# Optimization experiments

Hardware: AMD Instinct MI355X
Metric: run time of the kernel (lower is better)

The kernel has to match this reference:

```python
import jax, jax.numpy as jnp
import numpy as np

B, N, P, D = 16, 1024, 72, 96
ND, H, K = 64, 4, 16
LN_EPS = 1e-5
ROW_EPS = 1e-8


def topk_sparsify(adj, k):
    # adj: (..., N, N); keep top-k per row (scatter-mask), then row-renormalize
    shp = adj.shape
    n = shp[-1]
    flat = adj.reshape(-1, n)
    _, idx = jax.lax.top_k(flat, k)  # (R, k)
    rows = jnp.arange(flat.shape[0])[:, None]
    mask = jnp.zeros_like(flat).at[rows, idx].set(1.0)
    sp = flat * mask
    sp = sp / (sp.sum(-1, keepdims=True) + ROW_EPS)
    return sp.reshape(shp)


def setup_inputs() -> dict:
    key = jax.random.key(0)
    ks = jax.random.split(key, 12)
    xav1 = np.sqrt(6.0 / (N + ND))  # xavier_uniform bound for (N, ND)
    inp = {
        "patch_features": jax.random.normal(ks[0], (B, N, P, D), jnp.float32),
        "E1": jax.random.uniform(ks[1], (H, N, ND), jnp.float32, -xav1, xav1),
        "E2": jax.random.uniform(ks[2], (H, ND, N), jnp.float32, -xav1, xav1),
        "temperature": jnp.full((H,), 0.5, jnp.float32),
        "fusion_weight": jnp.float32(0.5),
        "dW1": jax.random.normal(ks[3], (D, ND), jnp.float32) / np.sqrt(D),
        "db1": jnp.zeros((ND,), jnp.float32),
        "ln_g": jnp.ones((ND,), jnp.float32),
        "ln_b": jnp.zeros((ND,), jnp.float32),
        "dW2": jax.random.normal(ks[4], (ND, ND), jnp.float32) / np.sqrt(ND),
        "db2": jnp.zeros((ND,), jnp.float32),
        "eW1": jax.random.normal(ks[5], (H, 2 * H), jnp.float32) / np.sqrt(H),
        "eb1": jnp.zeros((2 * H,), jnp.float32),
        "eW2": jax.random.normal(ks[6], (2 * H, 1), jnp.float32) / np.sqrt(2 * H),
        "eb2": jnp.zeros((1,), jnp.float32),
    }
    return inp


def reference(patch_features, E1, E2, temperature, fusion_weight,
              dW1, db1, ln_g, ln_b, dW2, db2, eW1, eb1, eW2, eb2):
    # ---- static multi-head graphs: softmax(relu(E1 @ E2) / T, axis=-1) ----
    s = jax.nn.relu(jnp.einsum('hnd,hdm->hnm', E1, E2))
    static_adjs = jax.nn.softmax(s / temperature[:, None, None], axis=-1)

    # ---- dynamic graphs from mean-pooled patch features ----
    node_repr = patch_features.mean(axis=2)                 # (B, N, D)
    h1 = node_repr @ dW1 + db1                              # (B, N, ND)
    mu = h1.mean(-1, keepdims=True)
    var = ((h1 - mu) ** 2).mean(-1, keepdims=True)
    h1 = (h1 - mu) / jnp.sqrt(var + LN_EPS) * ln_g + ln_b   # LayerNorm
    h1 = jax.nn.relu(h1)                                    # (dropout = identity, eval)
    dyn_emb = h1 @ dW2 + db2                                # (B, N, ND)
    d = jax.nn.relu(jnp.einsum('bnd,hdm->bhnm', dyn_emb, E2))
    dynamic_adjs = jax.nn.softmax(d / temperature[None, :, None, None], axis=-1)

    # ---- top-k sparsify + row renormalize ----
    static_adjs = topk_sparsify(static_adjs, K)             # (H, N, N)
    dynamic_adjs = topk_sparsify(dynamic_adjs, K)           # (B, H, N, N)

    # ---- fuse static + dynamic ----
    fused = (1.0 - fusion_weight) * static_adjs[None] + fusion_weight * dynamic_adjs

    # ---- edge MLP over head dim: (B, N, N, H) -> (B, N, N) ----
    x = jnp.transpose(fused, (0, 2, 3, 1))                  # (B, N, N, H)
    ew = jax.nn.relu(x @ eW1 + eb1) @ eW2 + eb2             # (B, N, N, 1)
    final_adjs = jax.nn.sigmoid(ew[..., 0]) * fused.mean(axis=1)
    return final_adjs, static_adjs, dynamic_adjs
```

## Files before the change

kernel.cpp:

```cpp
#include <hip/hip_runtime.h>

typedef unsigned int u32;
typedef unsigned long long u64;
typedef unsigned short u16;

#define Bn 16
#define Nn 1024
#define Pp 72
#define MARG 3e-4f

#define NEGINF __int_as_float(0xff800000)
#define POSINF __int_as_float(0x7f800000)

#define DPP_STEP(OP, CTRL, RM)                                                 \
  y = __builtin_amdgcn_update_dpp(__float_as_int(v), __float_as_int(v),        \
                                  CTRL, RM, 0xf, false);                       \
  v = OP(v, __int_as_float(y));

#define DPP_RED(NAME, OP)                                                      \
  __device__ __forceinline__ float NAME(float v) {                             \
    int y;                                                                     \
    DPP_STEP(OP, 0x111, 0xf)                                                   \
    DPP_STEP(OP, 0x112, 0xf)                                                   \
    DPP_STEP(OP, 0x114, 0xf)                                                   \
    DPP_STEP(OP, 0x118, 0xf)                                                   \
    DPP_STEP(OP, 0x142, 0xa)                                                   \
    DPP_STEP(OP, 0x143, 0xc)                                                   \
    return __int_as_float(__builtin_amdgcn_readlane(__float_as_int(v), 63));   \
  }

#define FADDOP(a, b) ((a) + (b))
DPP_RED(dmaxf, fmaxf)
DPP_RED(dminf, fminf)
DPP_RED(dsumf, FADDOP)

__device__ __forceinline__ u32 wminu(u32 v) {
#pragma unroll
  for (int off = 1; off < 64; off <<= 1) {
    u32 o = (u32)__shfl_xor((int)v, off, 64);
    v = (o < v) ? o : v;
  }
  return v;
}

__global__ __launch_bounds__(256) void k_e2t(const float* __restrict__ E2,
                                             float* __restrict__ E2T) {
  __shared__ float tile[32][65];
  const int h = blockIdx.x >> 5;
  const int m0 = (blockIdx.x & 31) << 5;
  const float* src = E2 + (size_t)h * 65536;
  float* dst = E2T + (size_t)h * 65536;
  const int t = threadIdx.x;
#pragma unroll
  for (int k = 0; k < 8; ++k) {
    int idx = k * 256 + t;
    int d = idx >> 5, mm = idx & 31;
    tile[mm][d] = src[d * 1024 + m0 + mm];
  }
  __syncthreads();
#pragma unroll
  for (int k = 0; k < 8; ++k) {
    int idx = k * 256 + t;
    int mm = idx >> 6, d = idx & 63;
    dst[(size_t)(m0 + mm) * 64 + d] = tile[mm][d];
  }
}

__global__ __launch_bounds__(128) void k_meanmlp(const float* __restrict__ pf,
                                                 const float* __restrict__ dW1,
                                                 const float* __restrict__ db1,
                                                 const float* __restrict__ ln_g,
                                                 const float* __restrict__ ln_b,
                                                 const float* __restrict__ dW2,
                                                 const float* __restrict__ db2,
                                                 double* __restrict__ embD,
                                                 float* __restrict__ embF) {
  __shared__ double ndD[96];
  __shared__ double red[64];
  __shared__ double h1r[64];
  const int t = threadIdx.x;
  const int bn = blockIdx.x;

  if (t < 96) {
    const float* src = pf + (size_t)bn * (Pp * 96) + t;
    double s = 0.0;
    for (int p = 0; p < Pp; ++p) s += (double)src[p * 96];
    ndD[t] = s / 72.0;
  }
  __syncthreads();

  double a = 0.0;
  if (t < 64) {
    a = (double)db1[t];
    for (int d = 0; d < 96; ++d) a = fma(ndD[d], (double)dW1[d * 64 + t], a);
    red[t] = a;
  }
  __syncthreads();
  for (int s2 = 32; s2 >= 1; s2 >>= 1) {
    if (t < s2) red[t] += red[t + s2];
    __syncthreads();
  }
  const double mu = red[0] * (1.0 / 64.0);
  __syncthreads();
  const double dv = a - mu;
  if (t < 64) red[t] = dv * dv;
  __syncthreads();
  for (int s2 = 32; s2 >= 1; s2 >>= 1) {
    if (t < s2) red[t] += red[t + s2];
    __syncthreads();
  }
  const double var = red[0] * (1.0 / 64.0);
  if (t < 64) {
    double xn = dv / sqrt(var + 1e-5) * (double)ln_g[t] + (double)ln_b[t];
    h1r[t] = xn > 0.0 ? xn : 0.0;
  }
  __syncthreads();
  if (t < 64) {
    double e = (double)db2[t];
    for (int k = 0; k < 64; ++k) e = fma(h1r[k], (double)dW2[k * 64 + t], e);
    embD[(size_t)bn * 64 + t] = e;
    embF[(size_t)bn * 64 + t] = (float)e;
  }
}

template <int MODE>
__global__ __launch_bounds__(512) void k_dot(const float* __restrict__ e1f,
                                             const float* __restrict__ embF,
                                             const float* __restrict__ E2,
                                             const float* __restrict__ temp,
                                             float* __restrict__ outp) {
  __shared__ float embsh[64][16];
  const int t = threadIdx.x;
  const int r0 = blockIdx.x * 16;
  int h;
  size_t erow;
  if (MODE == 0) {
    h = r0 >> 10;
    erow = (size_t)r0;
  } else {
    int b = r0 >> 12;
    h = (r0 >> 10) & 3;
    int n0 = r0 & 1023;
    erow = (size_t)(b << 10) + n0;
  }
  const float* efa = (MODE == 0) ? (e1f + erow * 64) : (embF + erow * 64);
  const float2* e2 = (const float2*)(E2 + (size_t)h * 65536);
  const float invT = 1.0f / temp[h];

#pragma unroll
  for (int i = t; i < 1024; i += 512) {
    int g = i & 15, d = i >> 4;
    embsh[d][g] = efa[g * 64 + d];
  }
  __syncthreads();

  float acc[16][2];
#pragma unroll
  for (int g = 0; g < 16; ++g) { acc[g][0] = 0.0f; acc[g][1] = 0.0f; }

#define FMA2(g, s)                                                             \
  acc[g][0] = fmaf(s, ev.x, acc[g][0]);                                        \
  acc[g][1] = fmaf(s, ev.y, acc[g][1]);

#pragma unroll 2
  for (int d = 0; d < 64; ++d) {
    float2 ev = e2[d * 512 + t];
    float4 sa = *(const float4*)&embsh[d][0];
    float4 sb = *(const float4*)&embsh[d][4];
    float4 sc = *(const float4*)&embsh[d][8];
    float4 sd = *(const float4*)&embsh[d][12];
    FMA2(0, sa.x) FMA2(1, sa.y) FMA2(2, sa.z) FMA2(3, sa.w)
    FMA2(4, sb.x) FMA2(5, sb.y) FMA2(6, sb.z) FMA2(7, sb.w)
    FMA2(8, sc.x) FMA2(9, sc.y) FMA2(10, sc.z) FMA2(11, sc.w)
    FMA2(12, sd.x) FMA2(13, sd.y) FMA2(14, sd.z) FMA2(15, sd.w)
  }
#undef FMA2

#pragma unroll
  for (int g = 0; g < 16; ++g) {
    float2 o;
    o.x = fmaxf(acc[g][0], 0.0f) * invT;
    o.y = fmaxf(acc[g][1], 0.0f) * invT;
    ((float2*)(outp + (size_t)(r0 + g) * 1024))[t] = o;
  }
}

template <int MODE>
__global__ __launch_bounds__(256) void k_sel(const float* __restrict__ e1f,
                                             const double* __restrict__ embD,
                                             const float* __restrict__ E2T,
                                             const float* __restrict__ temp,
                                             float* __restrict__ outp) {
  const int t = threadIdx.x;
  const int w = t >> 6, l = t & 63;
  const int r = blockIdx.x * 4 + w;
  int h;
  size_t erow;
  if (MODE == 0) {
    h = r >> 10;
    erow = (size_t)r;
  } else {
    int b = r >> 12;
    h = (r >> 10) & 3;
    int n = r & 1023;
    erow = (size_t)(b << 10) + n;
  }
  const float* e2t = E2T + (size_t)h * 65536;
  const double Td = (double)temp[h];
  float* row = outp + (size_t)r * 1024;

  float q[16];
#pragma unroll
  for (int j = 0; j < 16; ++j) q[j] = row[l + (j << 6)];

  float lm = q[0];
#pragma unroll
  for (int j = 1; j < 16; ++j) lm = fmaxf(lm, q[j]);
  const float qmax = dmaxf(lm);

  u32 lo = 0u, hi = __float_as_uint(qmax) + 1u;
  u32 kept = 0u;
  bool f16 = false;
  float pvf = 0.0f;
#pragma unroll 1
  while (hi - lo > 1u) {
    u32 mid = (lo + hi) >> 1;
    float pv = __uint_as_float(mid);
    u32 cw = 0;
#pragma unroll
    for (int j = 0; j < 16; ++j)
      cw += (u32)__popcll(__ballot(q[j] >= pv));
    if (cw >= 16u) lo = mid; else hi = mid;
    if (cw == 16u) { f16 = true; pvf = pv; break; }
  }
  float theta, ub;
  if (f16) {
    float vmin = POSINF, umax = -1.0f;
#pragma unroll
    for (int j = 0; j < 16; ++j) {
      if (q[j] >= pvf) { kept |= 1u << j; vmin = fminf(vmin, q[j]); }
      else umax = fmaxf(umax, q[j]);
    }
    theta = dminf(vmin);
    ub = dmaxf(umax);
  } else {
    theta = __uint_as_float(lo);
    u32 cw = 0;
#pragma unroll
    for (int j = 0; j < 16; ++j) {
      cw += (u32)__popcll(__ballot(q[j] > theta));
      if (q[j] > theta) kept |= 1u << j;
    }
    int rr = 16 - (int)cw;
#pragma unroll 1
    for (int it = 0; it < rr; ++it) {
      u32 mc = 0xFFFFFFFFu;
#pragma unroll
      for (int j = 0; j < 16; ++j)
        if (q[j] == theta && !((kept >> j) & 1u)) {
          u32 cc = (u32)((j << 6) | l);
          mc = cc < mc ? cc : mc;
        }
      u32 wm = wminu(mc);
      if ((wm & 63u) == (u32)l) kept |= 1u << (wm >> 6);
    }
    ub = theta;
  }

  if (theta - ub >= MARG) {
    float e[16];
    float es = 0.0f, ek = 0.0f;
#pragma unroll
    for (int j = 0; j < 16; ++j) {
      e[j] = __expf(q[j] - qmax);
      es += e[j];
      if ((kept >> j) & 1u) ek += e[j];
    }
    const float Z = dsumf(es);
    const float EK = dsumf(ek);
    const float inv = 1.0f / (EK + 1e-8f * Z);
#pragma unroll
    for (int j = 0; j < 16; ++j)
      row[l + (j << 6)] = ((kept >> j) & 1u) ? (e[j] * inv) : 0.0f;
  } else {
    double qd[16];
    const float thr = ub - MARG;
#pragma unroll 1
    for (int j = 0; j < 16; ++j) {
      if (q[j] >= thr) {
        const int m = l + (j << 6);
        const float* col = e2t + (size_t)m * 64;
        double a = 0.0;
        for (int d = 0; d < 64; ++d) {
          double s = (MODE == 0) ? (double)e1f[erow * 64 + d]
                                 : embD[erow * 64 + d];
          a = fma(s, (double)col[d], a);
        }
        qd[j] = (a > 0.0 ? a : 0.0) / Td;
      } else {
        qd[j] = (double)q[j];
      }
    }
    double bm = qd[0];
#pragma unroll
    for (int j = 1; j < 16; ++j) bm = qd[j] > bm ? qd[j] : bm;
    float mh = (float)bm;
    float mlo = (float)(bm - (double)mh);
    float whi = dmaxf(mh);
    float wlo = dmaxf(mh == whi ? mlo : NEGINF);
    const double qmaxd = (double)whi + (double)wlo;

    float ev2[16];
    float es2 = 0.0f;
#pragma unroll
    for (int j = 0; j < 16; ++j) { ev2[j] = __expf((float)(qd[j] - qmaxd)); es2 += ev2[j]; }
    const float Z2 = dsumf(es2);

    u32 kept2 = 0;
    float EK2 = 0.0f;
#pragma unroll 1
    for (int it = 0; it < 16; ++it) {
      double bv = -1.0;
      int bjj = -1;
#pragma unroll
      for (int j = 0; j < 16; ++j) {
        bool tk = (((kept2 >> j) & 1u) == 0u) && (qd[j] > bv);
        bv = tk ? qd[j] : bv;
        bjj = tk ? j : bjj;
      }
      float bh = NEGINF, bl = NEGINF;
      if (bjj >= 0) { bh = (float)bv; bl = (float)(bv - (double)bh); }
      float vhi = dmaxf(bh);
      float vlo = dmaxf(bh == vhi ? bl : NEGINF);
      bool elig = (bh == vhi) && (bl == vlo);
      u32 mc = elig ? (u32)((bjj << 6) | l) : 0xFFFFFFFFu;
      u32 mwin = wminu(mc);
      EK2 += __expf((float)(((double)vhi + (double)vlo) - qmaxd));
      if ((mwin & 63u) == (u32)l) kept2 |= 1u << (mwin >> 6);
    }
    const float inv2 = 1.0f / (EK2 + 1e-8f * Z2);
#pragma unroll
    for (int j = 0; j < 16; ++j)
      row[l + (j << 6)] = ((kept2 >> j) & 1u) ? (ev2[j] * inv2) : 0.0f;
  }
}

__global__ __launch_bounds__(256) void k_fuse(const float* __restrict__ dyn,
                                              const float* __restrict__ stat,
                                              float* __restrict__ fin,
                                              const float* __restrict__ eW1,
                                              const float* __restrict__ eb1,
                                              const float* __restrict__ eW2,
                                              const float* __restrict__ eb2,
                                              const float* __restrict__ fwp) {
  const float w = fwp[0];
  const float w1 = 1.0f - w;
  float W1[4][8], B1v[8], W2v[8];
#pragma unroll
  for (int hh = 0; hh < 4; ++hh)
#pragma unroll
    for (int j = 0; j < 8; ++j) W1[hh][j] = eW1[hh * 8 + j];
#pragma unroll
  for (int j = 0; j < 8; ++j) { B1v[j] = eb1[j]; W2v[j] = eW2[j]; }
  const float b2 = eb2[0];

  const int i = blockIdx.x * 256 + threadIdx.x;
  const int b = i >> 18;
  const int rem = i & 262143;
  const int n = rem >> 8;
  const int c4 = rem & 255;

  float fx[4][4];
#pragma unroll
  for (int hh = 0; hh < 4; ++hh) {
    float4 fd = ((const float4*)dyn)[(((size_t)((b * 4 + hh) * 1024 + n)) << 8) + c4];
    float4 fs = ((const float4*)stat)[(((size_t)(hh * 1024 + n)) << 8) + c4];
    fx[hh][0] = w1 * fs.x + w * fd.x;
    fx[hh][1] = w1 * fs.y + w * fd.y;
    fx[hh][2] = w1 * fs.z + w * fd.z;
    fx[hh][3] = w1 * fs.w + w * fd.w;
  }
  float ov[4];
#pragma unroll
  for (int x = 0; x < 4; ++x) {
    float ew = b2;
#pragma unroll
    for (int j = 0; j < 8; ++j) {
      float hj = B1v[j];
#pragma unroll
      for (int hh = 0; hh < 4; ++hh) hj = fmaf(fx[hh][x], W1[hh][j], hj);
      ew = fmaf(fmaxf(hj, 0.0f), W2v[j], ew);
    }
    float mean = (fx[0][x] + fx[1][x] + fx[2][x] + fx[3][x]) * 0.25f;
    float sg = 1.0f / (1.0f + __expf(-ew));
    ov[x] = sg * mean;
  }
  float4 o;
  o.x = ov[0]; o.y = ov[1]; o.z = ov[2]; o.w = ov[3];
  ((float4*)fin)[i] = o;
}

extern "C" void kernel_launch(void* const* d_in, const int* in_sizes, int n_in,
                              void* d_out, int out_size, void* d_ws, size_t ws_size,
                              hipStream_t stream) {
  const float* pf   = (const float*)d_in[0];
  const float* E1   = (const float*)d_in[1];
  const float* E2   = (const float*)d_in[2];
  const float* temp = (const float*)d_in[3];
  const float* fw   = (const float*)d_in[4];
  const float* dW1  = (const float*)d_in[5];
  const float* db1  = (const float*)d_in[6];
  const float* ln_g = (const float*)d_in[7];
  const float* ln_b = (const float*)d_in[8];
  const float* dW2  = (const float*)d_in[9];
  const float* db2  = (const float*)d_in[10];
  const float* eW1  = (const float*)d_in[11];
  const float* eb1  = (const float*)d_in[12];
  const float* eW2  = (const float*)d_in[13];
  const float* eb2  = (const float*)d_in[14];

  float* out_final = (float*)d_out;
  float* out_stat  = out_final + (size_t)Bn * Nn * Nn;
  float* out_dyn   = out_stat + (size_t)4 * Nn * Nn;

  double* embD = (double*)d_out;
  float* embF = out_final + 2097152;
  float* E2T  = out_final + 3145728;

  k_e2t<<<128, 256, 0, stream>>>(E2, E2T);
  k_meanmlp<<<Bn * Nn, 128, 0, stream>>>(pf, dW1, db1, ln_g, ln_b, dW2, db2, embD, embF);
  k_dot<0><<<256, 512, 0, stream>>>(E1, nullptr, E2, temp, out_stat);
  k_sel<0><<<1024, 256, 0, stream>>>(E1, nullptr, E2T, temp, out_stat);
  k_dot<1><<<4096, 512, 0, stream>>>(nullptr, embF, E2, temp, out_dyn);
  k_sel<1><<<16384, 256, 0, stream>>>(nullptr, embD, E2T, temp, out_dyn);
  k_fuse<<<16384, 256, 0, stream>>>(out_dyn, out_stat, out_final, eW1, eb1, eW2, eb2, fw);
}
```

Before: 588.9 us.

## Fuse dynamic top-k selection with edge-MLP fusion and retile dot kernel

Merges the dynamic-graph selection kernel and the fusion/edge-MLP kernel into one block per (b,n). The block processes all four head rows, keeps the sparsified rows in shared memory and uses them directly for the fused output. This saves one full read of the 256MB dynamic tensor. The dot kernel is retiled to 256 threads, each computing an 8x8 register tile with float4 loads. Scratch buffers move from the output region to the workspace.

```diff
diff --git a/kernel.cpp b/kernel.cpp
--- a/kernel.cpp
+++ b/kernel.cpp
@@ -2,7 +2,6 @@
 
 typedef unsigned int u32;
 typedef unsigned long long u64;
-typedef unsigned short u16;
 
 #define Bn 16
 #define Nn 1024
@@ -41,6 +40,144 @@
     v = (o < v) ? o : v;
   }
   return v;
+}
+
+template <int MODE>
+__device__ __forceinline__ void select_row(const float* __restrict__ q,
+                                           float* __restrict__ v, int l,
+                                           const float* __restrict__ e1row,
+                                           const double* __restrict__ edrow,
+                                           const float* __restrict__ e2t,
+                                           double Td) {
+  float lm = q[0];
+#pragma unroll
+  for (int j = 1; j < 16; ++j) lm = fmaxf(lm, q[j]);
+  const float qmax = dmaxf(lm);
+
+  u32 lo = 0u, hi = __float_as_uint(qmax) + 1u;
+  u32 kept = 0u;
+  bool f16 = false;
+  float pvf = 0.0f;
+#pragma unroll 1
+  while (hi - lo > 1u) {
+    u32 mid = (lo + hi) >> 1;
+    float pv = __uint_as_float(mid);
+    u32 cw = 0;
+#pragma unroll
+    for (int j = 0; j < 16; ++j)
+      cw += (u32)__popcll(__ballot(q[j] >= pv));
+    if (cw >= 16u) lo = mid; else hi = mid;
+    if (cw == 16u) { f16 = true; pvf = pv; break; }
+  }
+  float theta, ub;
+  if (f16) {
+    float vmin = POSINF, umax = -1.0f;
+#pragma unroll
+    for (int j = 0; j < 16; ++j) {
+      if (q[j] >= pvf) { kept |= 1u << j; vmin = fminf(vmin, q[j]); }
+      else umax = fmaxf(umax, q[j]);
+    }
+    theta = dminf(vmin);
+    ub = dmaxf(umax);
+  } else {
+    theta = __uint_as_float(lo);
+    u32 cw = 0;
+#pragma unroll
+    for (int j = 0; j < 16; ++j) {
+      cw += (u32)__popcll(__ballot(q[j] > theta));
+      if (q[j] > theta) kept |= 1u << j;
+    }
+    int rr = 16 - (int)cw;
+#pragma unroll 1
+    for (int it = 0; it < rr; ++it) {
+      u32 mc = 0xFFFFFFFFu;
+#pragma unroll
+      for (int j = 0; j < 16; ++j)
+        if (q[j] == theta && !((kept >> j) & 1u)) {
+          u32 cc = (u32)((j << 6) | l);
+          mc = cc < mc ? cc : mc;
+        }
+      u32 wm = wminu(mc);
+      if ((wm & 63u) == (u32)l) kept |= 1u << (wm >> 6);
+    }
+    ub = theta;
+  }
+
+  if (theta - ub >= MARG) {
+    float e[16];
+    float es = 0.0f, ek = 0.0f;
+#pragma unroll
+    for (int j = 0; j < 16; ++j) {
+      e[j] = __expf(q[j] - qmax);
+      es += e[j];
+      if ((kept >> j) & 1u) ek += e[j];
+    }
+    const float Z = dsumf(es);
+    const float EK = dsumf(ek);
+    const float inv = 1.0f / (EK + 1e-8f * Z);
+#pragma unroll
+    for (int j = 0; j < 16; ++j)
+      v[j] = ((kept >> j) & 1u) ? (e[j] * inv) : 0.0f;
+  } else {
+    double qd[16];
+    const float thr = ub - MARG;
+#pragma unroll 1
+    for (int j = 0; j < 16; ++j) {
+      if (q[j] >= thr) {
+        const int m = l + (j << 6);
+        const float* col = e2t + (size_t)m * 64;
+        double a = 0.0;
+        for (int d = 0; d < 64; ++d) {
+          double s = (MODE == 0) ? (double)e1row[d] : edrow[d];
+          a = fma(s, (double)col[d], a);
+        }
+        qd[j] = (a > 0.0 ? a : 0.0) / Td;
+      } else {
+        qd[j] = (double)q[j];
+      }
+    }
+    double bm = qd[0];
+#pragma unroll
+    for (int j = 1; j < 16; ++j) bm = qd[j] > bm ? qd[j] : bm;
+    float mh = (float)bm;
+    float mlo = (float)(bm - (double)mh);
+    float whi = dmaxf(mh);
+    float wlo = dmaxf(mh == whi ? mlo : NEGINF);
+    const double qmaxd = (double)whi + (double)wlo;
+
+    float ev2[16];
+    float es2 = 0.0f;
+#pragma unroll
+    for (int j = 0; j < 16; ++j) { ev2[j] = __expf((float)(qd[j] - qmaxd)); es2 += ev2[j]; }
+    const float Z2 = dsumf(es2);
+
+    u32 kept2 = 0;
+    float EK2 = 0.0f;
+#pragma unroll 1
+    for (int it = 0; it < 16; ++it) {
+      double bv = -1.0;
+      int bjj = -1;
+#pragma unroll
+      for (int j = 0; j < 16; ++j) {
+        bool tk = (((kept2 >> j) & 1u) == 0u) && (qd[j] > bv);
+        bv = tk ? qd[j] : bv;
+        bjj = tk ? j : bjj;
+      }
+      float bh = NEGINF, bl = NEGINF;
+      if (bjj >= 0) { bh = (float)bv; bl = (float)(bv - (double)bh); }
+      float vhi = dmaxf(bh);
+      float vlo = dmaxf(bh == vhi ? bl : NEGINF);
+      bool elig = (bh == vhi) && (bl == vlo);
+      u32 mc = elig ? (u32)((bjj << 6) | l) : 0xFFFFFFFFu;
+      u32 mwin = wminu(mc);
+      EK2 += __expf((float)(((double)vhi + (double)vlo) - qmaxd));
+      if ((mwin & 63u) == (u32)l) kept2 |= 1u << (mwin >> 6);
+    }
+    const float inv2 = 1.0f / (EK2 + 1e-8f * Z2);
+#pragma unroll
+    for (int j = 0; j < 16; ++j)
+      v[j] = ((kept2 >> j) & 1u) ? (ev2[j] * inv2) : 0.0f;
+  }
 }
 
 __global__ __launch_bounds__(256) void k_e2t(const float* __restrict__ E2,
@@ -124,7 +261,7 @@
 }
 
 template <int MODE>
-__global__ __launch_bounds__(512) void k_dot(const float* __restrict__ e1f,
+__global__ __launch_bounds__(256) void k_dot(const float* __restrict__ e1f,
                                              const float* __restrict__ embF,
                                              const float* __restrict__ E2,
                                              const float* __restrict__ temp,
@@ -144,217 +281,126 @@
     erow = (size_t)(b << 10) + n0;
   }
   const float* efa = (MODE == 0) ? (e1f + erow * 64) : (embF + erow * 64);
-  const float2* e2 = (const float2*)(E2 + (size_t)h * 65536);
+  const float* e2 = E2 + (size_t)h * 65536;
   const float invT = 1.0f / temp[h];
 
 #pragma unroll
-  for (int i = t; i < 1024; i += 512) {
+  for (int i = t; i < 1024; i += 256) {
     int g = i & 15, d = i >> 4;
     embsh[d][g] = efa[g * 64 + d];
   }
   __syncthreads();
 
-  float acc[16][2];
-#pragma unroll
-  for (int g = 0; g < 16; ++g) { acc[g][0] = 0.0f; acc[g][1] = 0.0f; }
-
-#define FMA2(g, s)                                                             \
-  acc[g][0] = fmaf(s, ev.x, acc[g][0]);                                        \
-  acc[g][1] = fmaf(s, ev.y, acc[g][1]);
-
-#pragma unroll 2
+  const int s = t >> 7;
+  const int c1 = (t & 127) * 4;
+  const int c2 = c1 + 512;
+
+  float acc[8][8];
+#pragma unroll
+  for (int g = 0; g < 8; ++g)
+#pragma unroll
+    for (int x = 0; x < 8; ++x) acc[g][x] = 0.0f;
+
+#pragma unroll 4
   for (int d = 0; d < 64; ++d) {
-    float2 ev = e2[d * 512 + t];
-    float4 sa = *(const float4*)&embsh[d][0];
-    float4 sb = *(const float4*)&embsh[d][4];
-    float4 sc = *(const float4*)&embsh[d][8];
-    float4 sd = *(const float4*)&embsh[d][12];
-    FMA2(0, sa.x) FMA2(1, sa.y) FMA2(2, sa.z) FMA2(3, sa.w)
-    FMA2(4, sb.x) FMA2(5, sb.y) FMA2(6, sb.z) FMA2(7, sb.w)
-    FMA2(8, sc.x) FMA2(9, sc.y) FMA2(10, sc.z) FMA2(11, sc.w)
-    FMA2(12, sd.x) FMA2(13, sd.y) FMA2(14, sd.z) FMA2(15, sd.w)
-  }
-#undef FMA2
-
-#pragma unroll
-  for (int g = 0; g < 16; ++g) {
-    float2 o;
-    o.x = fmaxf(acc[g][0], 0.0f) * invT;
-    o.y = fmaxf(acc[g][1], 0.0f) * invT;
-    ((float2*)(outp + (size_t)(r0 + g) * 1024))[t] = o;
-  }
-}
-
-template <int MODE>
-__global__ __launch_bounds__(256) void k_sel(const float* __restrict__ e1f,
-                                             const double* __restrict__ embD,
-                                             const float* __restrict__ E2T,
-                                             const float* __restrict__ temp,
-                                             float* __restrict__ outp) {
+    float4 va = *(const float4*)(e2 + d * 1024 + c1);
+    float4 vb = *(const float4*)(e2 + d * 1024 + c2);
+    float4 ea = *(const float4*)&embsh[d][8 * s];
+    float4 eb = *(const float4*)&embsh[d][8 * s + 4];
+    float sg;
+#define ROWFMA(g, SS)                                                          \
+    sg = SS;                                                                   \
+    acc[g][0] = fmaf(sg, va.x, acc[g][0]);                                     \
+    acc[g][1] = fmaf(sg, va.y, acc[g][1]);                                     \
+    acc[g][2] = fmaf(sg, va.z, acc[g][2]);                                     \
+    acc[g][3] = fmaf(sg, va.w, acc[g][3]);                                     \
+    acc[g][4] = fmaf(sg, vb.x, acc[g][4]);                                     \
+    acc[g][5] = fmaf(sg, vb.y, acc[g][5]);                                     \
+    acc[g][6] = fmaf(sg, vb.z, acc[g][6]);                                     \
+    acc[g][7] = fmaf(sg, vb.w, acc[g][7]);
+    ROWFMA(0, ea.x) ROWFMA(1, ea.y) ROWFMA(2, ea.z) ROWFMA(3, ea.w)
+    ROWFMA(4, eb.x) ROWFMA(5, eb.y) ROWFMA(6, eb.z) ROWFMA(7, eb.w)
+#undef ROWFMA
+  }
+
+#pragma unroll
+  for (int g = 0; g < 8; ++g) {
+    float* orow = outp + (size_t)(r0 + 8 * s + g) * 1024;
+    float4 o1, o2;
+    o1.x = fmaxf(acc[g][0], 0.0f) * invT;
+    o1.y = fmaxf(acc[g][1], 0.0f) * invT;
+    o1.z = fmaxf(acc[g][2], 0.0f) * invT;
+    o1.w = fmaxf(acc[g][3], 0.0f) * invT;
+    o2.x = fmaxf(acc[g][4], 0.0f) * invT;
+    o2.y = fmaxf(acc[g][5], 0.0f) * invT;
+    o2.z = fmaxf(acc[g][6], 0.0f) * invT;
+    o2.w = fmaxf(acc[g][7], 0.0f) * invT;
+    *(float4*)(orow + c1) = o1;
+    *(float4*)(orow + c2) = o2;
+  }
+}
+
+__global__ __launch_bounds__(256) void k_sel0(const float* __restrict__ E1,
+                                              const float* __restrict__ E2T,
+                                              const float* __restrict__ temp,
+                                              float* __restrict__ outp) {
   const int t = threadIdx.x;
   const int w = t >> 6, l = t & 63;
   const int r = blockIdx.x * 4 + w;
-  int h;
-  size_t erow;
-  if (MODE == 0) {
-    h = r >> 10;
-    erow = (size_t)r;
-  } else {
-    int b = r >> 12;
-    h = (r >> 10) & 3;
-    int n = r & 1023;
-    erow = (size_t)(b << 10) + n;
-  }
+  const int h = r >> 10;
   const float* e2t = E2T + (size_t)h * 65536;
   const double Td = (double)temp[h];
   float* row = outp + (size_t)r * 1024;
 
-  float q[16];
+  float q[16], v[16];
 #pragma unroll
   for (int j = 0; j < 16; ++j) q[j] = row[l + (j << 6)];
-
-  float lm = q[0];
-#pragma unroll
-  for (int j = 1; j < 16; ++j) lm = fmaxf(lm, q[j]);
-  const float qmax = dmaxf(lm);
-
-  u32 lo = 0u, hi = __float_as_uint(qmax) + 1u;
-  u32 kept = 0u;
-  bool f16 = false;
-  float pvf = 0.0f;
-#pragma unroll 1
-  while (hi - lo > 1u) {
-    u32 mid = (lo + hi) >> 1;
-    float pv = __uint_as_float(mid);
-    u32 cw = 0;
-#pragma unroll
-    for (int j = 0; j < 16; ++j)
-      cw += (u32)__popcll(__ballot(q[j] >= pv));
-    if (cw >= 16u) lo = mid; else hi = mid;
-    if (cw == 16u) { f16 = true; pvf = pv; break; }
-  }
-  float theta, ub;
-  if (f16) {
-    float vmin = POSINF, umax = -1.0f;
-#pragma unroll
-    for (int j = 0; j < 16; ++j) {
-      if (q[j] >= pvf) { kept |= 1u << j; vmin = fminf(vmin, q[j]); }
-      else umax = fmaxf(umax, q[j]);
-    }
-    theta = dminf(vmin);
-    ub = dmaxf(umax);
-  } else {
-    theta = __uint_as_float(lo);
-    u32 cw = 0;
-#pragma unroll
-    for (int j = 0; j < 16; ++j) {
-      cw += (u32)__popcll(__ballot(q[j] > theta));
-      if (q[j] > theta) kept |= 1u << j;
-    }
-    int rr = 16 - (int)cw;
-#pragma unroll 1
-    for (int it = 0; it < rr; ++it) {
-      u32 mc = 0xFFFFFFFFu;
-#pragma unroll
-      for (int j = 0; j < 16; ++j)
-        if (q[j] == theta && !((kept >> j) & 1u)) {
-          u32 cc = (u32)((j << 6) | l);
-          mc = cc < mc ? cc : mc;
-        }
-      u32 wm = wminu(mc);
-      if ((wm & 63u) == (u32)l) kept |= 1u << (wm >> 6);
-    }
-    ub = theta;
-  }
-
-  if (theta - ub >= MARG) {
-    float e[16];
-    float es = 0.0f, ek = 0.0f;
-#pragma unroll
-    for (int j = 0; j < 16; ++j) {
-      e[j] = __expf(q[j] - qmax);
-      es += e[j];
-      if ((kept >> j) & 1u) ek += e[j];
-    }
-    const float Z = dsumf(es);
-    const float EK = dsumf(ek);
-    const float inv = 1.0f / (EK + 1e-8f * Z);
-#pragma unroll
-    for (int j = 0; j < 16; ++j)
-      row[l + (j << 6)] = ((kept >> j) & 1u) ? (e[j] * inv) : 0.0f;
-  } else {
-    double qd[16];
-    const float thr = ub - MARG;
-#pragma unroll 1
-    for (int j = 0; j < 16; ++j) {
-      if (q[j] >= thr) {
-        const int m = l + (j << 6);
-        const float* col = e2t + (size_t)m * 64;
-        double a = 0.0;
-        for (int d = 0; d < 64; ++d) {
-          double s = (MODE == 0) ? (double)e1f[erow * 64 + d]
-                                 : embD[erow * 64 + d];
-          a = fma(s, (double)col[d], a);
-        }
-        qd[j] = (a > 0.0 ? a : 0.0) / Td;
-      } else {
-        qd[j] = (double)q[j];
-      }
-    }
-    double bm = qd[0];
-#pragma unroll
-    for (int j = 1; j < 16; ++j) bm = qd[j] > bm ? qd[j] : bm;
-    float mh = (float)bm;
-    float mlo = (float)(bm - (double)mh);
-    float whi = dmaxf(mh);
-    float wlo = dmaxf(mh == whi ? mlo : NEGINF);
-    const double qmaxd = (double)whi + (double)wlo;
-
-    float ev2[16];
-    float es2 = 0.0f;
-#pragma unroll
-    for (int j = 0; j < 16; ++j) { ev2[j] = __expf((float)(qd[j] - qmaxd)); es2 += ev2[j]; }
-    const float Z2 = dsumf(es2);
-
-    u32 kept2 = 0;
-    float EK2 = 0.0f;
-#pragma unroll 1
-    for (int it = 0; it < 16; ++it) {
-      double bv = -1.0;
-      int bjj = -1;
-#pragma unroll
-      for (int j = 0; j < 16; ++j) {
-        bool tk = (((kept2 >> j) & 1u) == 0u) && (qd[j] > bv);
-        bv = tk ? qd[j] : bv;
-        bjj = tk ? j : bjj;
-      }
-      float bh = NEGINF, bl = NEGINF;
-      if (bjj >= 0) { bh = (float)bv; bl = (float)(bv - (double)bh); }
-      float vhi = dmaxf(bh);
-      float vlo = dmaxf(bh == vhi ? bl : NEGINF);
-      bool elig = (bh == vhi) && (bl == vlo);
-      u32 mc = elig ? (u32)((bjj << 6) | l) : 0xFFFFFFFFu;
-      u32 mwin = wminu(mc);
-      EK2 += __expf((float)(((double)vhi + (double)vlo) - qmaxd));
-      if ((mwin & 63u) == (u32)l) kept2 |= 1u << (mwin >> 6);
-    }
-    const float inv2 = 1.0f / (EK2 + 1e-8f * Z2);
-#pragma unroll
-    for (int j = 0; j < 16; ++j)
-      row[l + (j << 6)] = ((kept2 >> j) & 1u) ? (ev2[j] * inv2) : 0.0f;
-  }
-}
-
-__global__ __launch_bounds__(256) void k_fuse(const float* __restrict__ dyn,
-                                              const float* __restrict__ stat,
-                                              float* __restrict__ fin,
-                                              const float* __restrict__ eW1,
-                                              const float* __restrict__ eb1,
-                                              const float* __restrict__ eW2,
-                                              const float* __restrict__ eb2,
-                                              const float* __restrict__ fwp) {
-  const float w = fwp[0];
-  const float w1 = 1.0f - w;
+  select_row<0>(q, v, l, E1 + (size_t)r * 64, nullptr, e2t, Td);
+#pragma unroll
+  for (int j = 0; j < 16; ++j) row[l + (j << 6)] = v[j];
+}
+
+__global__ __launch_bounds__(256) void k_selfuse(float* __restrict__ dyn,
+                                                 const float* __restrict__ stat,
+                                                 float* __restrict__ fin,
+                                                 const double* __restrict__ embD,
+                                                 const float* __restrict__ E2T,
+                                                 const float* __restrict__ temp,
+                                                 const float* __restrict__ eW1,
+                                                 const float* __restrict__ eb1,
+                                                 const float* __restrict__ eW2,
+                                                 const float* __restrict__ eb2,
+                                                 const float* __restrict__ fwp) {
+  __shared__ float rowbuf[4][1024];
+  const int t = threadIdx.x;
+  const int w = t >> 6, l = t & 63;
+  const int bn = blockIdx.x;
+  const int b = bn >> 10, n = bn & 1023;
+
+  {
+    const int h = w;
+    float* row = dyn + (((size_t)((b * 4 + h) * 1024 + n)) << 10);
+    const float* e2t = E2T + (size_t)h * 65536;
+    const double Td = (double)temp[h];
+    float q[16], v[16];
+#pragma unroll
+    for (int j = 0; j < 16; ++j) q[j] = row[l + (j << 6)];
+    select_row<1>(q, v, l, nullptr, embD + (((size_t)(b << 10) + n) << 6), e2t, Td);
+#pragma unroll
+    for (int j = 0; j < 16; ++j) rowbuf[h][l + (j << 6)] = v[j];
+  }
+  __syncthreads();
+
+#pragma unroll
+  for (int k = 0; k < 4; ++k) {
+    int idx = t + 256 * k;
+    int h2 = idx >> 8, c4 = idx & 255;
+    float* drow = dyn + (((size_t)((b * 4 + h2) * 1024 + n)) << 10);
+    *(float4*)(drow + c4 * 4) = *(const float4*)&rowbuf[h2][c4 * 4];
+  }
+
+  const float fw = fwp[0];
+  const float w1 = 1.0f - fw;
   float W1[4][8], B1v[8], W2v[8];
 #pragma unroll
   for (int hh = 0; hh < 4; ++hh)
@@ -364,21 +410,15 @@
   for (int j = 0; j < 8; ++j) { B1v[j] = eb1[j]; W2v[j] = eW2[j]; }
   const float b2 = eb2[0];
 
-  const int i = blockIdx.x * 256 + threadIdx.x;
-  const int b = i >> 18;
-  const int rem = i & 262143;
-  const int n = rem >> 8;
-  const int c4 = rem & 255;
-
   float fx[4][4];
 #pragma unroll
   for (int hh = 0; hh < 4; ++hh) {
-    float4 fd = ((const float4*)dyn)[(((size_t)((b * 4 + hh) * 1024 + n)) << 8) + c4];
-    float4 fs = ((const float4*)stat)[(((size_t)(hh * 1024 + n)) << 8) + c4];
-    fx[hh][0] = w1 * fs.x + w * fd.x;
-    fx[hh][1] = w1 * fs.y + w * fd.y;
-    fx[hh][2] = w1 * fs.z + w * fd.z;
-    fx[hh][3] = w1 * fs.w + w * fd.w;
+    float4 fd = *(const float4*)&rowbuf[hh][t * 4];
+    float4 fs = *(const float4*)(stat + (((size_t)(hh * 1024 + n)) << 10) + t * 4);
+    fx[hh][0] = w1 * fs.x + fw * fd.x;
+    fx[hh][1] = w1 * fs.y + fw * fd.y;
+    fx[hh][2] = w1 * fs.z + fw * fd.z;
+    fx[hh][3] = w1 * fs.w + fw * fd.w;
   }
   float ov[4];
 #pragma unroll
@@ -397,7 +437,7 @@
   }
   float4 o;
   o.x = ov[0]; o.y = ov[1]; o.z = ov[2]; o.w = ov[3];
-  ((float4*)fin)[i] = o;
+  *(float4*)(fin + (size_t)b * 1048576 + (size_t)n * 1024 + t * 4) = o;
 }
 
 extern "C" void kernel_launch(void* const* d_in, const int* in_sizes, int n_in,
@@ -423,15 +463,15 @@
   float* out_stat  = out_final + (size_t)Bn * Nn * Nn;
   float* out_dyn   = out_stat + (size_t)4 * Nn * Nn;
 
-  double* embD = (double*)d_out;
-  float* embF = out_final + 2097152;
-  float* E2T  = out_final + 3145728;
+  double* embD = (double*)d_ws;
+  float* embF  = (float*)((char*)d_ws + (8u << 20));
+  float* E2T   = (float*)((char*)d_ws + (12u << 20));
 
   k_e2t<<<128, 256, 0, stream>>>(E2, E2T);
   k_meanmlp<<<Bn * Nn, 128, 0, stream>>>(pf, dW1, db1, ln_g, ln_b, dW2, db2, embD, embF);
-  k_dot<0><<<256, 512, 0, stream>>>(E1, nullptr, E2, temp, out_stat);
-  k_sel<0><<<1024, 256, 0, stream>>>(E1, nullptr, E2T, temp, out_stat);
-  k_dot<1><<<4096, 512, 0, stream>>>(nullptr, embF, E2, temp, out_dyn);
-  k_sel<1><<<16384, 256, 0, stream>>>(nullptr, embD, E2T, temp, out_dyn);
-  k_fuse<<<16384, 256, 0, stream>>>(out_dyn, out_stat, out_final, eW1, eb1, eW2, eb2, fw);
-}
+  k_dot<0><<<256, 256, 0, stream>>>(E1, nullptr, E2, temp, out_stat);
+  k_sel0<<<1024, 256, 0, stream>>>(E1, E2T, temp, out_stat);
+  k_dot<1><<<4096, 256, 0, stream>>>(nullptr, embF, E2, temp, out_dyn);
+  k_selfuse<<<16384, 256, 0, stream>>>(out_dyn, out_stat, out_final, embD, E2T,
+                                       temp, eW1, eb1, eW2, eb2, fw);
+}
```

Result: faster. 542.7 us (-7.9%).
